# Performance work log

Measured on AMD Instinct MI355X. Metric: run time of the kernel, lower is better.

Reference implementation:

```python
import jax, jax.numpy as jnp
import numpy as np

B, S, IN, OUT = 4, 2048, 4096, 4096


def setup_inputs() -> dict:
    key = jax.random.key(0)
    k1, k2 = jax.random.split(key, 2)
    x = jax.random.normal(k1, (B, S, IN), dtype=jnp.float32)
    # Materialize the quantized weight the way bitsandbytes int8_vectorwise_quant does:
    # per-output-row absmax (SCB) and int8 codes CB = round(W * 127 / absmax_row).
    Wf = jax.random.normal(k2, (OUT, IN), dtype=jnp.float32) * 0.02
    absmax = jnp.max(jnp.abs(Wf), axis=1)  # [OUT]
    CB = jnp.round(Wf * (127.0 / absmax)[:, None]).astype(jnp.int8)  # [OUT, IN]
    SCB = absmax.astype(jnp.float32)  # [OUT], per-row absmax scale
    return {"x": x, "CB": CB, "SCB": SCB}


def reference(x, CB, SCB):
    # LLM.int8()-style forward (has_fp16_weights=False, no outlier split needed for
    # well-behaved activations): dynamic row-wise int8 quantization of x, int8 GEMM
    # accumulated in int32, then dequant by (absmax_x/127) * (SCB/127).
    absmax_x = jnp.max(jnp.abs(x), axis=-1, keepdims=True)  # [B,S,1]
    sx = absmax_x / 127.0
    xq = jnp.round(x / sx).astype(jnp.int8)  # [B,S,IN]
    acc = jnp.einsum("bsk,ok->bso", xq, CB, preferred_element_type=jnp.int32)
    y = acc.astype(jnp.float32) * sx * (SCB / 127.0)[None, None, :]  # [B,S,OUT]
    return y
```

## Files before the change

### kernel.cpp

```cpp
#include <hip/hip_runtime.h>
#include <stdint.h>

static constexpr int Mtot = 8192;
static constexpr int Ntot = 4096;
static constexpr int Ktot = 4096;

using i32x4 = __attribute__((ext_vector_type(4))) int;

#define GLD16(gptr, lptr)                                                                   \
  __builtin_amdgcn_global_load_lds((const __attribute__((address_space(1))) void*)(gptr),   \
                                   (__attribute__((address_space(3))) void*)(lptr), 16, 0, 0)
#define WAITVM(N) asm volatile("s_waitcnt vmcnt(" #N ")" ::: "memory")

__global__ __launch_bounds__(256) void prep_kernel(const int* __restrict__ cb32,
                                                   int8_t* __restrict__ cb8,
                                                   const float* __restrict__ x,
                                                   int8_t* __restrict__ xq,
                                                   float* __restrict__ sx) {
  __shared__ float wmax[4];
  if (blockIdx.x < 16384) {
    const int idx = blockIdx.x * 256 + threadIdx.x;
    const int4 v = reinterpret_cast<const int4*>(cb32)[idx];
    const unsigned packed = (unsigned)(v.x & 0xff) | ((unsigned)(v.y & 0xff) << 8) |
                            ((unsigned)(v.z & 0xff) << 16) | ((unsigned)(v.w & 0xff) << 24);
    reinterpret_cast<unsigned*>(cb8)[idx] = packed;
    return;
  }
  const int row = blockIdx.x - 16384;
  const float4* xr = reinterpret_cast<const float4*>(x + (size_t)row * Ktot);
  float4 v[4];
  float am = 0.f;
#pragma unroll
  for (int i = 0; i < 4; ++i) {
    v[i] = xr[threadIdx.x + i * 256];
    am = fmaxf(am, fmaxf(fmaxf(fabsf(v[i].x), fabsf(v[i].y)),
                         fmaxf(fabsf(v[i].z), fabsf(v[i].w))));
  }
#pragma unroll
  for (int off = 32; off > 0; off >>= 1) am = fmaxf(am, __shfl_xor(am, off));
  if ((threadIdx.x & 63) == 0) wmax[threadIdx.x >> 6] = am;
  __syncthreads();
  am = fmaxf(fmaxf(wmax[0], wmax[1]), fmaxf(wmax[2], wmax[3]));
  const float inv = 127.0f / am;
  if (threadIdx.x == 0) sx[row] = am * (1.0f / 127.0f);
  unsigned* dq = reinterpret_cast<unsigned*>(xq + (size_t)row * Ktot);
#pragma unroll
  for (int i = 0; i < 4; ++i) {
    const int q0 = (int)rintf(v[i].x * inv);
    const int q1 = (int)rintf(v[i].y * inv);
    const int q2 = (int)rintf(v[i].z * inv);
    const int q3 = (int)rintf(v[i].w * inv);
    dq[threadIdx.x + i * 256] = (unsigned)(q0 & 0xff) | ((unsigned)(q1 & 0xff) << 8) |
                                ((unsigned)(q2 & 0xff) << 16) | ((unsigned)(q3 & 0xff) << 24);
  }
}

__global__ __launch_bounds__(512, 2) void gemm_i8_kernel(const int8_t* __restrict__ A,
                                                         const int8_t* __restrict__ B,
                                                         const float* __restrict__ sx,
                                                         const float* __restrict__ scb,
                                                         float* __restrict__ C) {
  constexpr int BK = 128;
  constexpr int NT = Ktot / BK;
  __shared__ __align__(16) int8_t lds[131072];

  const int tid = threadIdx.x;
  const int lane = tid & 63;
  const int wid = tid >> 6;

  const int wg = (int)blockIdx.x;
  const int wgs = (wg & 7) * 64 + (wg >> 3);
  const int m0 = (wgs >> 4) * 256;
  const int n0 = (wgs & 15) * 256;

  const int wm = (wid >> 2) * 128;
  const int wn = (wid & 3) * 64;

  const int srow = tid >> 3;
  const int scol = ((tid & 7) * 16) ^ ((srow & 7) << 4);
  const int8_t* gA = A + (size_t)(m0 + srow) * Ktot + scol;
  const int8_t* gB = B + (size_t)(n0 + srow) * Ktot + scol;

  const int l15 = lane & 15;
  const int lc0 = ((lane >> 4) * 16) ^ ((lane & 7) << 4);
  const int aOff = (wm + l15) * 128 + lc0;
  const int bOff = 65536 + (wn + l15) * 128 + lc0;

  i32x4 acc[8][4];
#pragma unroll
  for (int f = 0; f < 8; ++f)
#pragma unroll
    for (int g = 0; g < 4; ++g) acc[f][g] = (i32x4)0;

#pragma unroll
  for (int i = 0; i < 4; ++i) GLD16(gB + (size_t)(i * 64) * Ktot, &lds[65536 + i * 8192 + tid * 16]);
  GLD16(gA + (size_t)(0 * 64) * Ktot, &lds[0 * 8192 + tid * 16]);
  GLD16(gA + (size_t)(2 * 64) * Ktot, &lds[2 * 8192 + tid * 16]);
  GLD16(gA + (size_t)(1 * 64) * Ktot, &lds[1 * 8192 + tid * 16]);
  GLD16(gA + (size_t)(3 * 64) * Ktot, &lds[3 * 8192 + tid * 16]);
  WAITVM(2);
  __builtin_amdgcn_s_barrier();

  for (int t = 0; t < NT - 1; ++t) {
    const int bo = (t & 1) * 32768;
    const int so = bo ^ 32768;
    const size_t kn = (size_t)(t + 1) * BK;
    i32x4 a[4], b[4];

#pragma unroll
    for (int f = 0; f < 4; ++f) a[f] = *(const i32x4*)&lds[bo + aOff + f * 2048];
#pragma unroll
    for (int g = 0; g < 4; ++g) b[g] = *(const i32x4*)&lds[bo + bOff + g * 2048];
#pragma unroll
    for (int i = 0; i < 4; ++i)
      GLD16(gB + kn + (size_t)(i * 64) * Ktot, &lds[65536 + so + i * 8192 + tid * 16]);
    __builtin_amdgcn_s_barrier();
    __builtin_amdgcn_s_setprio(1);
#pragma unroll
    for (int f = 0; f < 4; ++f)
#pragma unroll
      for (int g = 0; g < 4; ++g)
        acc[f][g] = __builtin_amdgcn_mfma_i32_16x16x64_i8(a[f], b[g], acc[f][g], 0, 0, 0);
    __builtin_amdgcn_s_setprio(0);
    WAITVM(4);
    __builtin_amdgcn_s_barrier();

#pragma unroll
    for (int f = 0; f < 4; ++f) a[f] = *(const i32x4*)&lds[bo + aOff + (f + 4) * 2048];
    __builtin_amdgcn_s_barrier();
    __builtin_amdgcn_s_setprio(1);
#pragma unroll
    for (int f = 0; f < 4; ++f)
#pragma unroll
      for (int g = 0; g < 4; ++g)
        acc[f + 4][g] = __builtin_amdgcn_mfma_i32_16x16x64_i8(a[f], b[g], acc[f + 4][g], 0, 0, 0);
    __builtin_amdgcn_s_setprio(0);
    __builtin_amdgcn_s_barrier();

#pragma unroll
    for (int f = 0; f < 4; ++f) a[f] = *(const i32x4*)&lds[bo + (aOff ^ 64) + f * 2048];
#pragma unroll
    for (int g = 0; g < 4; ++g) b[g] = *(const i32x4*)&lds[bo + (bOff ^ 64) + g * 2048];
    GLD16(gA + kn + (size_t)(0 * 64) * Ktot, &lds[so + 0 * 8192 + tid * 16]);
    GLD16(gA + kn + (size_t)(2 * 64) * Ktot, &lds[so + 2 * 8192 + tid * 16]);
    GLD16(gA + kn + (size_t)(1 * 64) * Ktot, &lds[so + 1 * 8192 + tid * 16]);
    GLD16(gA + kn + (size_t)(3 * 64) * Ktot, &lds[so + 3 * 8192 + tid * 16]);
    __builtin_amdgcn_s_barrier();
    __builtin_amdgcn_s_setprio(1);
#pragma unroll
    for (int f = 0; f < 4; ++f)
#pragma unroll
      for (int g = 0; g < 4; ++g)
        acc[f][g] = __builtin_amdgcn_mfma_i32_16x16x64_i8(a[f], b[g], acc[f][g], 0, 0, 0);
    __builtin_amdgcn_s_setprio(0);
    __builtin_amdgcn_s_barrier();

#pragma unroll
    for (int f = 0; f < 4; ++f) a[f] = *(const i32x4*)&lds[bo + (aOff ^ 64) + (f + 4) * 2048];
    __builtin_amdgcn_s_barrier();
    __builtin_amdgcn_s_setprio(1);
#pragma unroll
    for (int f = 0; f < 4; ++f)
#pragma unroll
      for (int g = 0; g < 4; ++g)
        acc[f + 4][g] = __builtin_amdgcn_mfma_i32_16x16x64_i8(a[f], b[g], acc[f + 4][g], 0, 0, 0);
    __builtin_amdgcn_s_setprio(0);
    WAITVM(2);
    __builtin_amdgcn_s_barrier();
  }

  {
    const int bo = ((NT - 1) & 1) * 32768;
    i32x4 a[4], b[4];
#pragma unroll
    for (int f = 0; f < 4; ++f) a[f] = *(const i32x4*)&lds[bo + aOff + f * 2048];
#pragma unroll
    for (int g = 0; g < 4; ++g) b[g] = *(const i32x4*)&lds[bo + bOff + g * 2048];
    __builtin_amdgcn_s_barrier();
    __builtin_amdgcn_s_setprio(1);
#pragma unroll
    for (int f = 0; f < 4; ++f)
#pragma unroll
      for (int g = 0; g < 4; ++g)
        acc[f][g] = __builtin_amdgcn_mfma_i32_16x16x64_i8(a[f], b[g], acc[f][g], 0, 0, 0);
    __builtin_amdgcn_s_setprio(0);
    WAITVM(0);
    __builtin_amdgcn_s_barrier();

#pragma unroll
    for (int f = 0; f < 4; ++f) a[f] = *(const i32x4*)&lds[bo + aOff + (f + 4) * 2048];
    __builtin_amdgcn_s_barrier();
    __builtin_amdgcn_s_setprio(1);
#pragma unroll
    for (int f = 0; f < 4; ++f)
#pragma unroll
      for (int g = 0; g < 4; ++g)
        acc[f + 4][g] = __builtin_amdgcn_mfma_i32_16x16x64_i8(a[f], b[g], acc[f + 4][g], 0, 0, 0);
    __builtin_amdgcn_s_setprio(0);
    __builtin_amdgcn_s_barrier();

#pragma unroll
    for (int f = 0; f < 4; ++f) a[f] = *(const i32x4*)&lds[bo + (aOff ^ 64) + f * 2048];
#pragma unroll
    for (int g = 0; g < 4; ++g) b[g] = *(const i32x4*)&lds[bo + (bOff ^ 64) + g * 2048];
    __builtin_amdgcn_s_barrier();
    __builtin_amdgcn_s_setprio(1);
#pragma unroll
    for (int f = 0; f < 4; ++f)
#pragma unroll
      for (int g = 0; g < 4; ++g)
        acc[f][g] = __builtin_amdgcn_mfma_i32_16x16x64_i8(a[f], b[g], acc[f][g], 0, 0, 0);
    __builtin_amdgcn_s_setprio(0);
    __builtin_amdgcn_s_barrier();

#pragma unroll
    for (int f = 0; f < 4; ++f) a[f] = *(const i32x4*)&lds[bo + (aOff ^ 64) + (f + 4) * 2048];
    __builtin_amdgcn_s_setprio(1);
#pragma unroll
    for (int f = 0; f < 4; ++f)
#pragma unroll
      for (int g = 0; g < 4; ++g)
        acc[f + 4][g] = __builtin_amdgcn_mfma_i32_16x16x64_i8(a[f], b[g], acc[f + 4][g], 0, 0, 0);
    __builtin_amdgcn_s_setprio(0);
  }

  const int col = lane & 15;
  const int rbase = (lane >> 4) * 4;
#pragma unroll
  for (int f = 0; f < 8; ++f) {
    const int gmb = m0 + wm + f * 16 + rbase;
    float sm[4];
#pragma unroll
    for (int r = 0; r < 4; ++r) sm[r] = sx[gmb + r];
#pragma unroll
    for (int g = 0; g < 4; ++g) {
      const int gn = n0 + wn + g * 16 + col;
      const float snv = scb[gn] * (1.0f / 127.0f);
#pragma unroll
      for (int r = 0; r < 4; ++r)
        C[(size_t)(gmb + r) * Ntot + gn] = (float)acc[f][g][r] * sm[r] * snv;
    }
  }
}

extern "C" void kernel_launch(void* const* d_in, const int* in_sizes, int n_in,
                              void* d_out, int out_size, void* d_ws, size_t ws_size,
                              hipStream_t stream) {
  const float* x = (const float*)d_in[0];
  const int* CB32 = (const int*)d_in[1];
  const float* SCB = (const float*)d_in[2];
  float* out = (float*)d_out;

  int8_t* xq = (int8_t*)d_ws;
  int8_t* cb8 = (int8_t*)d_ws + (size_t)Mtot * Ktot;
  float* sx = (float*)((int8_t*)d_ws + (size_t)Mtot * Ktot + (size_t)Ntot * Ktot);

  prep_kernel<<<16384 + Mtot, 256, 0, stream>>>(CB32, cb8, x, xq, sx);
  gemm_i8_kernel<<<512, 512, 0, stream>>>(xq, cb8, sx, SCB, out);
}
```

Measured before the change: 385.3 us.

## Software-pipeline LDS fragment loads one MFMA phase ahead and cut barriers

Restructures the int8 GEMM main loop so that the LDS reads for the next MFMA phase (the other K-half and the other M-half) go into separate register sets and are issued before the current phase's MFMAs. The aim is to hide LDS read latency behind matrix math and to cut the number of barriers per iteration from eight to four. It also prefetches the first fragments before the loop and unrolls the loop by two. In exchange it needs more VGPRs for the double-buffered fragments, which risks lower occupancy or spills. The ordering of LDS reads against the async global-to-LDS writes also needs care.

New measurement: 376.0 us. 2.4% less time.

```diff
diff --git a/kernel.cpp b/kernel.cpp
--- a/kernel.cpp
+++ b/kernel.cpp
@@ -92,6 +92,8 @@
 #pragma unroll
     for (int g = 0; g < 4; ++g) acc[f][g] = (i32x4)0;
 
+  i32x4 aE[4], aO[4], b0v[4], b1v[4];
+
 #pragma unroll
   for (int i = 0; i < 4; ++i) GLD16(gB + (size_t)(i * 64) * Ktot, &lds[65536 + i * 8192 + tid * 16]);
   GLD16(gA + (size_t)(0 * 64) * Ktot, &lds[0 * 8192 + tid * 16]);
@@ -100,127 +102,114 @@
   GLD16(gA + (size_t)(3 * 64) * Ktot, &lds[3 * 8192 + tid * 16]);
   WAITVM(2);
   __builtin_amdgcn_s_barrier();
-
+#pragma unroll
+  for (int f = 0; f < 4; ++f) aE[f] = *(const i32x4*)&lds[aOff + f * 2048];
+#pragma unroll
+  for (int g = 0; g < 4; ++g) b0v[g] = *(const i32x4*)&lds[bOff + g * 2048];
+
+#pragma unroll 2
   for (int t = 0; t < NT - 1; ++t) {
     const int bo = (t & 1) * 32768;
     const int so = bo ^ 32768;
     const size_t kn = (size_t)(t + 1) * BK;
-    i32x4 a[4], b[4];
-
-#pragma unroll
-    for (int f = 0; f < 4; ++f) a[f] = *(const i32x4*)&lds[bo + aOff + f * 2048];
-#pragma unroll
-    for (int g = 0; g < 4; ++g) b[g] = *(const i32x4*)&lds[bo + bOff + g * 2048];
+
 #pragma unroll
     for (int i = 0; i < 4; ++i)
       GLD16(gB + kn + (size_t)(i * 64) * Ktot, &lds[65536 + so + i * 8192 + tid * 16]);
-    __builtin_amdgcn_s_barrier();
-    __builtin_amdgcn_s_setprio(1);
-#pragma unroll
-    for (int f = 0; f < 4; ++f)
-#pragma unroll
-      for (int g = 0; g < 4; ++g)
-        acc[f][g] = __builtin_amdgcn_mfma_i32_16x16x64_i8(a[f], b[g], acc[f][g], 0, 0, 0);
-    __builtin_amdgcn_s_setprio(0);
     WAITVM(4);
-    __builtin_amdgcn_s_barrier();
-
-#pragma unroll
-    for (int f = 0; f < 4; ++f) a[f] = *(const i32x4*)&lds[bo + aOff + (f + 4) * 2048];
-    __builtin_amdgcn_s_barrier();
-    __builtin_amdgcn_s_setprio(1);
-#pragma unroll
-    for (int f = 0; f < 4; ++f)
-#pragma unroll
-      for (int g = 0; g < 4; ++g)
-        acc[f + 4][g] = __builtin_amdgcn_mfma_i32_16x16x64_i8(a[f], b[g], acc[f + 4][g], 0, 0, 0);
-    __builtin_amdgcn_s_setprio(0);
-    __builtin_amdgcn_s_barrier();
-
-#pragma unroll
-    for (int f = 0; f < 4; ++f) a[f] = *(const i32x4*)&lds[bo + (aOff ^ 64) + f * 2048];
-#pragma unroll
-    for (int g = 0; g < 4; ++g) b[g] = *(const i32x4*)&lds[bo + (bOff ^ 64) + g * 2048];
+#pragma unroll
+    for (int f = 0; f < 4; ++f) aO[f] = *(const i32x4*)&lds[bo + (aOff ^ 64) + f * 2048];
+#pragma unroll
+    for (int g = 0; g < 4; ++g) b1v[g] = *(const i32x4*)&lds[bo + (bOff ^ 64) + g * 2048];
+    __builtin_amdgcn_s_setprio(1);
+#pragma unroll
+    for (int f = 0; f < 4; ++f)
+#pragma unroll
+      for (int g = 0; g < 4; ++g)
+        acc[f][g] = __builtin_amdgcn_mfma_i32_16x16x64_i8(aE[f], b0v[g], acc[f][g], 0, 0, 0);
+    __builtin_amdgcn_s_setprio(0);
+    __builtin_amdgcn_s_barrier();
+
     GLD16(gA + kn + (size_t)(0 * 64) * Ktot, &lds[so + 0 * 8192 + tid * 16]);
     GLD16(gA + kn + (size_t)(2 * 64) * Ktot, &lds[so + 2 * 8192 + tid * 16]);
     GLD16(gA + kn + (size_t)(1 * 64) * Ktot, &lds[so + 1 * 8192 + tid * 16]);
     GLD16(gA + kn + (size_t)(3 * 64) * Ktot, &lds[so + 3 * 8192 + tid * 16]);
-    __builtin_amdgcn_s_barrier();
-    __builtin_amdgcn_s_setprio(1);
-#pragma unroll
-    for (int f = 0; f < 4; ++f)
-#pragma unroll
-      for (int g = 0; g < 4; ++g)
-        acc[f][g] = __builtin_amdgcn_mfma_i32_16x16x64_i8(a[f], b[g], acc[f][g], 0, 0, 0);
-    __builtin_amdgcn_s_setprio(0);
-    __builtin_amdgcn_s_barrier();
-
-#pragma unroll
-    for (int f = 0; f < 4; ++f) a[f] = *(const i32x4*)&lds[bo + (aOff ^ 64) + (f + 4) * 2048];
-    __builtin_amdgcn_s_barrier();
-    __builtin_amdgcn_s_setprio(1);
-#pragma unroll
-    for (int f = 0; f < 4; ++f)
-#pragma unroll
-      for (int g = 0; g < 4; ++g)
-        acc[f + 4][g] = __builtin_amdgcn_mfma_i32_16x16x64_i8(a[f], b[g], acc[f + 4][g], 0, 0, 0);
+#pragma unroll
+    for (int f = 0; f < 4; ++f) aE[f] = *(const i32x4*)&lds[bo + aOff + (f + 4) * 2048];
+    __builtin_amdgcn_s_setprio(1);
+#pragma unroll
+    for (int f = 0; f < 4; ++f)
+#pragma unroll
+      for (int g = 0; g < 4; ++g)
+        acc[f][g] = __builtin_amdgcn_mfma_i32_16x16x64_i8(aO[f], b1v[g], acc[f][g], 0, 0, 0);
+    __builtin_amdgcn_s_setprio(0);
+    __builtin_amdgcn_s_barrier();
+
+#pragma unroll
+    for (int f = 0; f < 4; ++f) aO[f] = *(const i32x4*)&lds[bo + (aOff ^ 64) + (f + 4) * 2048];
+    __builtin_amdgcn_s_setprio(1);
+#pragma unroll
+    for (int f = 0; f < 4; ++f)
+#pragma unroll
+      for (int g = 0; g < 4; ++g)
+        acc[f + 4][g] = __builtin_amdgcn_mfma_i32_16x16x64_i8(aE[f], b0v[g], acc[f + 4][g], 0, 0, 0);
     __builtin_amdgcn_s_setprio(0);
     WAITVM(2);
+    __builtin_amdgcn_s_barrier();
+
+#pragma unroll
+    for (int f = 0; f < 4; ++f) aE[f] = *(const i32x4*)&lds[so + aOff + f * 2048];
+#pragma unroll
+    for (int g = 0; g < 4; ++g) b0v[g] = *(const i32x4*)&lds[so + bOff + g * 2048];
+    __builtin_amdgcn_s_setprio(1);
+#pragma unroll
+    for (int f = 0; f < 4; ++f)
+#pragma unroll
+      for (int g = 0; g < 4; ++g)
+        acc[f + 4][g] = __builtin_amdgcn_mfma_i32_16x16x64_i8(aO[f], b1v[g], acc[f + 4][g], 0, 0, 0);
+    __builtin_amdgcn_s_setprio(0);
     __builtin_amdgcn_s_barrier();
   }
 
   {
     const int bo = ((NT - 1) & 1) * 32768;
-    i32x4 a[4], b[4];
-#pragma unroll
-    for (int f = 0; f < 4; ++f) a[f] = *(const i32x4*)&lds[bo + aOff + f * 2048];
-#pragma unroll
-    for (int g = 0; g < 4; ++g) b[g] = *(const i32x4*)&lds[bo + bOff + g * 2048];
-    __builtin_amdgcn_s_barrier();
-    __builtin_amdgcn_s_setprio(1);
-#pragma unroll
-    for (int f = 0; f < 4; ++f)
-#pragma unroll
-      for (int g = 0; g < 4; ++g)
-        acc[f][g] = __builtin_amdgcn_mfma_i32_16x16x64_i8(a[f], b[g], acc[f][g], 0, 0, 0);
-    __builtin_amdgcn_s_setprio(0);
     WAITVM(0);
-    __builtin_amdgcn_s_barrier();
-
-#pragma unroll
-    for (int f = 0; f < 4; ++f) a[f] = *(const i32x4*)&lds[bo + aOff + (f + 4) * 2048];
-    __builtin_amdgcn_s_barrier();
-    __builtin_amdgcn_s_setprio(1);
-#pragma unroll
-    for (int f = 0; f < 4; ++f)
-#pragma unroll
-      for (int g = 0; g < 4; ++g)
-        acc[f + 4][g] = __builtin_amdgcn_mfma_i32_16x16x64_i8(a[f], b[g], acc[f + 4][g], 0, 0, 0);
-    __builtin_amdgcn_s_setprio(0);
-    __builtin_amdgcn_s_barrier();
-
-#pragma unroll
-    for (int f = 0; f < 4; ++f) a[f] = *(const i32x4*)&lds[bo + (aOff ^ 64) + f * 2048];
-#pragma unroll
-    for (int g = 0; g < 4; ++g) b[g] = *(const i32x4*)&lds[bo + (bOff ^ 64) + g * 2048];
-    __builtin_amdgcn_s_barrier();
-    __builtin_amdgcn_s_setprio(1);
-#pragma unroll
-    for (int f = 0; f < 4; ++f)
-#pragma unroll
-      for (int g = 0; g < 4; ++g)
-        acc[f][g] = __builtin_amdgcn_mfma_i32_16x16x64_i8(a[f], b[g], acc[f][g], 0, 0, 0);
-    __builtin_amdgcn_s_setprio(0);
-    __builtin_amdgcn_s_barrier();
-
-#pragma unroll
-    for (int f = 0; f < 4; ++f) a[f] = *(const i32x4*)&lds[bo + (aOff ^ 64) + (f + 4) * 2048];
-    __builtin_amdgcn_s_setprio(1);
-#pragma unroll
-    for (int f = 0; f < 4; ++f)
-#pragma unroll
-      for (int g = 0; g < 4; ++g)
-        acc[f + 4][g] = __builtin_amdgcn_mfma_i32_16x16x64_i8(a[f], b[g], acc[f + 4][g], 0, 0, 0);
+#pragma unroll
+    for (int f = 0; f < 4; ++f) aO[f] = *(const i32x4*)&lds[bo + (aOff ^ 64) + f * 2048];
+#pragma unroll
+    for (int g = 0; g < 4; ++g) b1v[g] = *(const i32x4*)&lds[bo + (bOff ^ 64) + g * 2048];
+    __builtin_amdgcn_s_setprio(1);
+#pragma unroll
+    for (int f = 0; f < 4; ++f)
+#pragma unroll
+      for (int g = 0; g < 4; ++g)
+        acc[f][g] = __builtin_amdgcn_mfma_i32_16x16x64_i8(aE[f], b0v[g], acc[f][g], 0, 0, 0);
+    __builtin_amdgcn_s_setprio(0);
+    __builtin_amdgcn_s_barrier();
+#pragma unroll
+    for (int f = 0; f < 4; ++f) aE[f] = *(const i32x4*)&lds[bo + aOff + (f + 4) * 2048];
+    __builtin_amdgcn_s_setprio(1);
+#pragma unroll
+    for (int f = 0; f < 4; ++f)
+#pragma unroll
+      for (int g = 0; g < 4; ++g)
+        acc[f][g] = __builtin_amdgcn_mfma_i32_16x16x64_i8(aO[f], b1v[g], acc[f][g], 0, 0, 0);
+    __builtin_amdgcn_s_setprio(0);
+#pragma unroll
+    for (int f = 0; f < 4; ++f) aO[f] = *(const i32x4*)&lds[bo + (aOff ^ 64) + (f + 4) * 2048];
+    __builtin_amdgcn_s_setprio(1);
+#pragma unroll
+    for (int f = 0; f < 4; ++f)
+#pragma unroll
+      for (int g = 0; g < 4; ++g)
+        acc[f + 4][g] = __builtin_amdgcn_mfma_i32_16x16x64_i8(aE[f], b0v[g], acc[f + 4][g], 0, 0, 0);
+    __builtin_amdgcn_s_setprio(0);
+    __builtin_amdgcn_s_setprio(1);
+#pragma unroll
+    for (int f = 0; f < 4; ++f)
+#pragma unroll
+      for (int g = 0; g < 4; ++g)
+        acc[f + 4][g] = __builtin_amdgcn_mfma_i32_16x16x64_i8(aO[f], b1v[g], acc[f + 4][g], 0, 0, 0);
     __builtin_amdgcn_s_setprio(0);
   }
 
```
